# Optimization experiments

Measured on AMD Instinct MI355X. Metric: run time of the kernel, lower is better.

## Reference

```python
import jax, jax.numpy as jnp
import numpy as np

D_MODEL = 1024
NUM_HEADS = 16
LN_EPS = 1e-5


def setup_inputs() -> dict:
    key = jax.random.key(0)
    ks = jax.random.split(key, 8)
    d = D_MODEL
    x = jax.random.normal(ks[0], (8, 1024, d), dtype=jnp.float32)
    # nn.MultiheadAttention parameters (combined in_proj, out_proj)
    in_proj_w = jax.random.normal(ks[1], (3 * d, d), dtype=jnp.float32) / np.sqrt(d)
    in_proj_b = jnp.zeros((3 * d,), dtype=jnp.float32)
    out_proj_w = jax.random.normal(ks[2], (d, d), dtype=jnp.float32) / np.sqrt(d)
    out_proj_b = jnp.zeros((d,), dtype=jnp.float32)
    ln_w = jnp.ones((d,), dtype=jnp.float32)
    ln_b = jnp.zeros((d,), dtype=jnp.float32)
    time_decay = jnp.asarray(0.1, dtype=jnp.float32)
    return {"x": x, "time_decay": time_decay, "in_proj_w": in_proj_w,
            "in_proj_b": in_proj_b, "out_proj_w": out_proj_w,
            "out_proj_b": out_proj_b, "ln_w": ln_w, "ln_b": ln_b}


def reference(x, time_decay, in_proj_w, in_proj_b, out_proj_w, out_proj_b, ln_w, ln_b):
    B, S, d = x.shape
    H = NUM_HEADS
    hd = d // H
    # vectorized time-decay bias: -|time_decay| * |i - j|  (replaces nested loop)
    idx = jnp.arange(S, dtype=jnp.float32)
    attn_bias = -jnp.abs(time_decay) * jnp.abs(idx[:, None] - idx[None, :])  # [S,S]
    # combined QKV projection
    qkv = x @ in_proj_w.T + in_proj_b  # [B,S,3d]
    q, k, v = jnp.split(qkv, 3, axis=-1)
    q = q.reshape(B, S, H, hd)
    k = k.reshape(B, S, H, hd)
    v = v.reshape(B, S, H, hd)
    scale = 1.0 / np.sqrt(hd)
    scores = jnp.einsum('bqhd,bkhd->bhqk', q, k) * scale + attn_bias  # [B,H,S,S]
    weights = jax.nn.softmax(scores, axis=-1)
    attn = jnp.einsum('bhqk,bkhd->bqhd', weights, v).reshape(B, S, d)
    attn_out = attn @ out_proj_w.T + out_proj_b
    # need_weights=True with default average_attn_weights=True -> mean over heads
    attn_weights = jnp.mean(weights, axis=1)  # [B,S,S]
    # residual + LayerNorm
    y = x + attn_out
    mu = jnp.mean(y, axis=-1, keepdims=True)
    var = jnp.mean(jnp.square(y - mu), axis=-1, keepdims=True)
    out = (y - mu) / jnp.sqrt(var + LN_EPS) * ln_w + ln_b
    return (out, attn_weights)
```

## Files before the change

kernel.cpp:

```cpp
#include <hip/hip_runtime.h>
#include <cstddef>

#define BATCH   8
#define SEQ     1024
#define DMODEL  1024
#define NHEAD   16
#define HDIM    64
#define D3      3072
#define NROWS   (BATCH * SEQ)
#define LN_EPS  1e-5f

typedef __attribute__((ext_vector_type(4))) float f32x4;
typedef __attribute__((ext_vector_type(8))) short bf16x8;

__device__ __forceinline__ float b2f(unsigned short u) {
    union { unsigned int i; float f; } v; v.i = ((unsigned int)u) << 16; return v.f;
}
__device__ __forceinline__ unsigned short f2bu(float f) {
    union { float f; unsigned int i; } v; v.f = f;
    unsigned int r = v.i + 0x7fffu + ((v.i >> 16) & 1u);
    return (unsigned short)(r >> 16);
}
__device__ __forceinline__ void gl16(const void* g, void* l) {
    __builtin_amdgcn_global_load_lds(
        (const __attribute__((address_space(1))) unsigned int*)g,
        (__attribute__((address_space(3))) unsigned int*)l, 16, 0, 0);
}

#define NG_X  1048576
#define NG_WQ 393216
#define NG_WO 131072
__global__ __launch_bounds__(256)
void cvt_bf16(const float* __restrict__ x, const float* __restrict__ wq,
              const float* __restrict__ wo,
              unsigned short* __restrict__ xb, unsigned short* __restrict__ wqb,
              unsigned short* __restrict__ wob) {
    const int gidx = blockIdx.x * 256 + threadIdx.x;
    const float* src; unsigned short* dst; size_t off;
    if (gidx < NG_X)              { src = x;  dst = xb;  off = (size_t)gidx * 8; }
    else if (gidx < NG_X + NG_WQ) { src = wq; dst = wqb; off = (size_t)(gidx - NG_X) * 8; }
    else                          { src = wo; dst = wob; off = (size_t)(gidx - NG_X - NG_WQ) * 8; }
    float4 v0 = *(const float4*)(src + off);
    float4 v1 = *(const float4*)(src + off + 4);
    uint4 pv;
    pv.x = f2bu(v0.x) | ((unsigned int)f2bu(v0.y) << 16);
    pv.y = f2bu(v0.z) | ((unsigned int)f2bu(v0.w) << 16);
    pv.z = f2bu(v1.x) | ((unsigned int)f2bu(v1.y) << 16);
    pv.w = f2bu(v1.z) | ((unsigned int)f2bu(v1.w) << 16);
    *(uint4*)(dst + off) = pv;
}

__global__ __launch_bounds__(256)
void qkv_mfma(const unsigned short* __restrict__ xb,
              const unsigned short* __restrict__ wb,
              const float* __restrict__ bias,
              unsigned short* __restrict__ qh,
              unsigned short* __restrict__ kh,
              unsigned short* __restrict__ vt) {
    __shared__ unsigned short smem[8192];
    unsigned short* As = smem;
    unsigned short* Bs = smem + 4096;

    const int t = threadIdx.x;
    const int w = t >> 6, lane = t & 63;
    const int wm = w >> 1, wn = w & 1;
    const int g = lane >> 4, c = lane & 15;
    const int m0 = blockIdx.y * 128, n0 = blockIdx.x * 128;

    const int srow = t >> 2;
    const int scol = (t & 3) * 8;
    const unsigned short* ga = xb + (size_t)(m0 + srow) * 1024 + scol;
    const unsigned short* gb = wb + (size_t)(n0 + srow) * 1024 + scol;

    f32x4 acc[4][4];
#pragma unroll
    for (int i = 0; i < 4; ++i)
#pragma unroll
        for (int j = 0; j < 4; ++j) acc[i][j] = (f32x4){0.f, 0.f, 0.f, 0.f};

    for (int k0 = 0; k0 < 1024; k0 += 32) {
        gl16(ga + k0,             As + t * 8);
        gl16(ga + 64 * 1024 + k0, As + 2048 + t * 8);
        gl16(gb + k0,             Bs + t * 8);
        gl16(gb + 64 * 1024 + k0, Bs + 2048 + t * 8);
        __syncthreads();
        bf16x8 af[4], bf[4];
#pragma unroll
        for (int i = 0; i < 4; ++i)
            af[i] = *(const bf16x8*)(As + (wm * 64 + i * 16 + c) * 32 + g * 8);
#pragma unroll
        for (int j = 0; j < 4; ++j)
            bf[j] = *(const bf16x8*)(Bs + (wn * 64 + j * 16 + c) * 32 + g * 8);
#pragma unroll
        for (int i = 0; i < 4; ++i)
#pragma unroll
            for (int j = 0; j < 4; ++j)
                acc[i][j] = __builtin_amdgcn_mfma_f32_16x16x32_bf16(af[i], bf[j], acc[i][j], 0, 0, 0);
        __syncthreads();
    }

    float bsv[4];
#pragma unroll
    for (int j = 0; j < 4; ++j) bsv[j] = bias[n0 + wn * 64 + j * 16 + c];

    unsigned short* eslice = smem + w * 2048;
    const int b_ = m0 >> 10;

    if (n0 < 2048) {
        const int ncl   = n0 + wn * 64;
        unsigned short* dst = (ncl < 1024)
            ? qh + ((size_t)(b_ * 16 + (ncl >> 6)) * 1024) * 64
            : kh + ((size_t)(b_ * 16 + ((ncl - 1024) >> 6)) * 1024) * 64;
#pragma unroll
        for (int half = 0; half < 2; ++half) {
#pragma unroll
            for (int ii = 0; ii < 2; ++ii) {
                const int i = half * 2 + ii;
#pragma unroll
                for (int j = 0; j < 4; ++j)
#pragma unroll
                    for (int r = 0; r < 4; ++r)
                        eslice[(ii * 16 + g * 4 + r) * 64 + j * 16 + c] = f2bu(acc[i][j][r] + bsv[j]);
            }
#pragma unroll
            for (int u = 0; u < 4; ++u) {
                const int mloc = u * 8 + (lane >> 3);
                const int ncol = (lane & 7) * 8;
                bf16x8 row = *(const bf16x8*)(eslice + mloc * 64 + ncol);
                const int tok = (m0 & 1023) + wm * 64 + half * 32 + mloc;
                *(bf16x8*)(dst + (size_t)tok * 64 + ncol) = row;
            }
        }
    } else {
        const int key0  = (m0 & 1023) + wm * 64;
        const int hbase = (n0 + wn * 64 - 2048) >> 6;
#pragma unroll
        for (int half = 0; half < 2; ++half) {
#pragma unroll
            for (int jj = 0; jj < 2; ++jj) {
                const int j = half * 2 + jj;
                const int nloc = jj * 16 + c;
#pragma unroll
                for (int i = 0; i < 4; ++i)
#pragma unroll
                    for (int r = 0; r < 4; ++r) {
                        const int mloc  = i * 16 + g * 4 + r;
                        const int mphys = mloc ^ ((nloc & 7) << 3);
                        eslice[nloc * 64 + mphys] = f2bu(acc[i][j][r] + bsv[j]);
                    }
            }
#pragma unroll
            for (int u = 0; u < 4; ++u) {
                const int nloc  = u * 8 + (lane >> 3);
                const int mb    = lane & 7;
                const int mphys = (mb ^ (nloc & 7)) * 8;
                bf16x8 row = *(const bf16x8*)(eslice + nloc * 64 + mphys);
                const int d = half * 32 + nloc;
                *(bf16x8*)(vt + ((size_t)((b_ * 16 + hbase) * 64 + d)) * 1024 + key0 + mb * 8) = row;
            }
        }
    }
}

__global__ __launch_bounds__(256, 1)
void attn_mfma(const unsigned short* __restrict__ qh,
               const unsigned short* __restrict__ kh,
               const unsigned short* __restrict__ vt,
               const float* __restrict__ tdp,
               unsigned short* __restrict__ attnb,
               float* __restrict__ wout) {
    const int qt = blockIdx.x;
    const int b  = blockIdx.y;
    const int hg = blockIdx.z;
    const int t  = threadIdx.x;
    const int w  = t >> 6;
    const int lane = t & 63;
    const int g  = lane >> 4;
    const int c  = lane & 15;

    const int q0 = qt * 64;
    const float td2 = -fabsf(tdp[0]) * 1.44269504f;
    const float sc2 = 0.125f * 1.44269504f;

    __shared__ unsigned short P_s[64][1032];
    __shared__ float rs_s[4][64];

    float wsum[4][16][4];
#pragma unroll
    for (int i = 0; i < 4; ++i)
#pragma unroll
        for (int tt = 0; tt < 16; ++tt)
#pragma unroll
            for (int r = 0; r < 4; ++r) wsum[i][tt][r] = 0.f;

    const int key_base = w * 256;
    const float kf0 = (float)(key_base + c);

    for (int hi = 0; hi < 8; ++hi) {
        const int h = hg * 8 + hi;
        const unsigned short* qslab = qh + (size_t)(b * 16 + h) * 1024 * 64;
        const unsigned short* kslab = kh + (size_t)(b * 16 + h) * 1024 * 64;

        bf16x8 qa[4][2];
#pragma unroll
        for (int i = 0; i < 4; ++i) {
            const unsigned short* qp = qslab + (size_t)(q0 + i * 16 + c) * 64 + g * 8;
            qa[i][0] = *(const bf16x8*)(qp);
            qa[i][1] = *(const bf16x8*)(qp + 32);
        }

        float rsum[4][4];
#pragma unroll
        for (int i = 0; i < 4; ++i)
#pragma unroll
            for (int r = 0; r < 4; ++r) rsum[i][r] = 0.f;

#pragma unroll 2
        for (int tt = 0; tt < 16; ++tt) {
            const int key = key_base + tt * 16 + c;
            const unsigned short* kp = kslab + (size_t)key * 64 + g * 8;
            bf16x8 kb0 = *(const bf16x8*)(kp);
            bf16x8 kb1 = *(const bf16x8*)(kp + 32);
            f32x4 z[4];
#pragma unroll
            for (int i = 0; i < 4; ++i) z[i] = (f32x4){0.f, 0.f, 0.f, 0.f};
#pragma unroll
            for (int i = 0; i < 4; ++i)
                z[i] = __builtin_amdgcn_mfma_f32_16x16x32_bf16(qa[i][0], kb0, z[i], 0, 0, 0);
#pragma unroll
            for (int i = 0; i < 4; ++i)
                z[i] = __builtin_amdgcn_mfma_f32_16x16x32_bf16(qa[i][1], kb1, z[i], 0, 0, 0);
            const float kf = kf0 + (float)(tt * 16);
#pragma unroll
            for (int i = 0; i < 4; ++i) {
#pragma unroll
                for (int r = 0; r < 4; ++r) {
                    const float qf = (float)(q0 + i * 16 + g * 4 + r);
                    const float e = __builtin_amdgcn_exp2f(z[i][r] * sc2 + td2 * fabsf(kf - qf));
                    rsum[i][r] += e;
                    P_s[i * 16 + g * 4 + r][key_base + tt * 16 + c] = f2bu(e);
                }
            }
        }
#pragma unroll
        for (int i = 0; i < 4; ++i)
#pragma unroll
            for (int r = 0; r < 4; ++r) {
                rsum[i][r] += __shfl_xor(rsum[i][r], 1, 64);
                rsum[i][r] += __shfl_xor(rsum[i][r], 2, 64);
                rsum[i][r] += __shfl_xor(rsum[i][r], 4, 64);
                rsum[i][r] += __shfl_xor(rsum[i][r], 8, 64);
            }
        if (c == 0) {
#pragma unroll
            for (int i = 0; i < 4; ++i)
#pragma unroll
                for (int r = 0; r < 4; ++r) rs_s[w][i * 16 + g * 4 + r] = rsum[i][r];
        }
        __syncthreads();

        float invl[4][4];
#pragma unroll
        for (int i = 0; i < 4; ++i)
#pragma unroll
            for (int r = 0; r < 4; ++r) {
                const int row = i * 16 + g * 4 + r;
                invl[i][r] = 1.0f / (rs_s[0][row] + rs_s[1][row] + rs_s[2][row] + rs_s[3][row]);
            }

        f32x4 accO[4];
#pragma unroll
        for (int i = 0; i < 4; ++i) accO[i] = (f32x4){0.f, 0.f, 0.f, 0.f};
        const unsigned short* vhp = vt + (size_t)((b * 16 + h) * 64 + w * 16 + c) * 1024;
#pragma unroll 4
        for (int ks = 0; ks < 32; ++ks) {
            bf16x8 vb = *(const bf16x8*)(vhp + ks * 32 + g * 8);
#pragma unroll
            for (int i = 0; i < 4; ++i) {
                bf16x8 pa = *(const bf16x8*)(&P_s[i * 16 + c][ks * 32 + g * 8]);
                accO[i] = __builtin_amdgcn_mfma_f32_16x16x32_bf16(pa, vb, accO[i], 0, 0, 0);
            }
        }
        {
            unsigned short* op = attnb + (size_t)(b * 1024 + q0) * 1024 + h * 64 + w * 16 + c;
#pragma unroll
            for (int i = 0; i < 4; ++i)
#pragma unroll
                for (int r = 0; r < 4; ++r)
                    op[(size_t)(i * 16 + g * 4 + r) * 1024] = f2bu(accO[i][r] * invl[i][r]);
        }

#pragma unroll
        for (int i = 0; i < 4; ++i)
#pragma unroll
            for (int tt = 0; tt < 16; ++tt)
#pragma unroll
                for (int r = 0; r < 4; ++r)
                    wsum[i][tt][r] += b2f(P_s[i * 16 + g * 4 + r][key_base + tt * 16 + c]) * invl[i][r];
        __syncthreads();
    }

#pragma unroll
    for (int i = 0; i < 4; ++i)
#pragma unroll
        for (int tt = 0; tt < 16; ++tt)
#pragma unroll
            for (int r = 0; r < 4; ++r) {
                atomicAdd(&wout[(size_t)(b * 1024 + q0 + i * 16 + g * 4 + r) * 1024
                                 + key_base + tt * 16 + c],
                          wsum[i][tt][r] * (1.0f / NHEAD));
            }
}

__global__ __launch_bounds__(256)
void outproj_mfma(const unsigned short* __restrict__ ab,
                  const unsigned short* __restrict__ wob,
                  const float* __restrict__ bias,
                  const float* __restrict__ X,
                  float* __restrict__ Y) {
    __shared__ unsigned short smem[8192];
    unsigned short* As = smem;
    unsigned short* Bs = smem + 4096;

    const int t = threadIdx.x;
    const int w = t >> 6, lane = t & 63;
    const int wm = w >> 1, wn = w & 1;
    const int g = lane >> 4, c = lane & 15;
    const int m0 = blockIdx.y * 128, n0 = blockIdx.x * 128;

    const int srow = t >> 2;
    const int scol = (t & 3) * 8;
    const unsigned short* ga = ab  + (size_t)(m0 + srow) * 1024 + scol;
    const unsigned short* gb = wob + (size_t)(n0 + srow) * 1024 + scol;

    f32x4 acc[4][4];
#pragma unroll
    for (int i = 0; i < 4; ++i)
#pragma unroll
        for (int j = 0; j < 4; ++j) acc[i][j] = (f32x4){0.f, 0.f, 0.f, 0.f};

    for (int k0 = 0; k0 < 1024; k0 += 32) {
        gl16(ga + k0,             As + t * 8);
        gl16(ga + 64 * 1024 + k0, As + 2048 + t * 8);
        gl16(gb + k0,             Bs + t * 8);
        gl16(gb + 64 * 1024 + k0, Bs + 2048 + t * 8);
        __syncthreads();
        bf16x8 af[4], bf[4];
#pragma unroll
        for (int i = 0; i < 4; ++i)
            af[i] = *(const bf16x8*)(As + (wm * 64 + i * 16 + c) * 32 + g * 8);
#pragma unroll
        for (int j = 0; j < 4; ++j)
            bf[j] = *(const bf16x8*)(Bs + (wn * 64 + j * 16 + c) * 32 + g * 8);
#pragma unroll
        for (int i = 0; i < 4; ++i)
#pragma unroll
            for (int j = 0; j < 4; ++j)
                acc[i][j] = __builtin_amdgcn_mfma_f32_16x16x32_bf16(af[i], bf[j], acc[i][j], 0, 0, 0);
        __syncthreads();
    }

    float bsv[4];
#pragma unroll
    for (int j = 0; j < 4; ++j) bsv[j] = bias[n0 + wn * 64 + j * 16 + c];

#pragma unroll
    for (int i = 0; i < 4; ++i) {
#pragma unroll
        for (int r = 0; r < 4; ++r) {
            const int m = m0 + wm * 64 + i * 16 + g * 4 + r;
#pragma unroll
            for (int j = 0; j < 4; ++j) {
                const int n = n0 + wn * 64 + j * 16 + c;
                Y[(size_t)m * 1024 + n] = acc[i][j][r] + bsv[j] + X[(size_t)m * 1024 + n];
            }
        }
    }
}

__global__ __launch_bounds__(256)
void ln_kernel(const float* __restrict__ Y, const float* __restrict__ lnw,
               const float* __restrict__ lnb, float* __restrict__ out) {
    const int row = blockIdx.x, t = threadIdx.x;
    __shared__ float rs[256], rq[256];
    const float4 v = ((const float4*)(Y + (size_t)row * DMODEL))[t];
    rs[t] = v.x + v.y + v.z + v.w;
    rq[t] = v.x * v.x + v.y * v.y + v.z * v.z + v.w * v.w;
    __syncthreads();
    for (int off = 128; off > 0; off >>= 1) {
        if (t < off) { rs[t] += rs[t + off]; rq[t] += rq[t + off]; }
        __syncthreads();
    }
    const float mu   = rs[0] * (1.0f / DMODEL);
    const float var  = rq[0] * (1.0f / DMODEL) - mu * mu;
    const float rstd = rsqrtf(var + LN_EPS);
    const float4 w  = ((const float4*)lnw)[t];
    const float4 bb = ((const float4*)lnb)[t];
    float4 o;
    o.x = (v.x - mu) * rstd * w.x + bb.x;
    o.y = (v.y - mu) * rstd * w.y + bb.y;
    o.z = (v.z - mu) * rstd * w.z + bb.z;
    o.w = (v.w - mu) * rstd * w.w + bb.w;
    ((float4*)(out + (size_t)row * DMODEL))[t] = o;
}

extern "C" void kernel_launch(void* const* d_in, const int* in_sizes, int n_in,
                              void* d_out, int out_size, void* d_ws, size_t ws_size,
                              hipStream_t stream) {
    (void)in_sizes; (void)n_in; (void)out_size; (void)ws_size;
    const float* x    = (const float*)d_in[0];
    const float* td   = (const float*)d_in[1];
    const float* wqkv = (const float*)d_in[2];
    const float* bqkv = (const float*)d_in[3];
    const float* wo   = (const float*)d_in[4];
    const float* bo   = (const float*)d_in[5];
    const float* lnw  = (const float*)d_in[6];
    const float* lnb  = (const float*)d_in[7];

    float* out_ln = (float*)d_out;
    float* out_w  = (float*)d_out + (size_t)NROWS * SEQ;

    unsigned short* qh = (unsigned short*)d_ws;
    unsigned short* kh = qh + (size_t)128 * 1024 * 64;
    unsigned short* vt = kh + (size_t)128 * 1024 * 64;
    float*          y  = (float*)d_ws;

    unsigned short* attnb = (unsigned short*)d_out;
    unsigned short* wob   = (unsigned short*)d_out + (size_t)NROWS * DMODEL;
    unsigned short* xb    = (unsigned short*)out_w;
    unsigned short* wqkvb = xb + (size_t)NROWS * DMODEL;

    cvt_bf16    <<<(NG_X + NG_WQ + NG_WO) / 256, 256, 0, stream>>>(x, wqkv, wo, xb, wqkvb, wob);
    qkv_mfma    <<<dim3(D3 / 128, NROWS / 128), 256, 0, stream>>>(xb, wqkvb, bqkv, qh, kh, vt);
    (void)hipMemsetAsync(out_w, 0, (size_t)BATCH * SEQ * SEQ * sizeof(float), stream);
    attn_mfma   <<<dim3(SEQ / 64, BATCH, 2),    256, 0, stream>>>(qh, kh, vt, td, attnb, out_w);
    outproj_mfma<<<dim3(DMODEL / 128, NROWS / 128), 256, 0, stream>>>(attnb, wob, bo, x, y);
    ln_kernel   <<<NROWS,                       256, 0, stream>>>(y, lnw, lnb, out_ln);
}
```

Baseline: 483.3 us.

## Use 8 waves per attention block with split-K PV and LDS reduction

The attention kernel moves from 256 to 512 threads per block. Each wave now covers 128 keys instead of 256, which halves the per-thread wsum register array. For the PV product, waves split the key dimension into two halves and combine their partial outputs through an LDS reduction buffer. The goal is more waves in flight and lower register pressure, at the cost of extra syncthreads, extra LDS, and the reduction step.

```diff
diff --git a/kernel.cpp b/kernel.cpp
--- a/kernel.cpp
+++ b/kernel.cpp
@@ -162,7 +162,7 @@
     }
 }
 
-__global__ __launch_bounds__(256, 1)
+__global__ __launch_bounds__(512, 2)
 void attn_mfma(const unsigned short* __restrict__ qh,
                const unsigned short* __restrict__ kh,
                const unsigned short* __restrict__ vt,
@@ -183,17 +183,19 @@
     const float sc2 = 0.125f * 1.44269504f;
 
     __shared__ unsigned short P_s[64][1032];
-    __shared__ float rs_s[4][64];
-
-    float wsum[4][16][4];
+    __shared__ float rs_s[8][64];
+    __shared__ float rs_tot[64];
+    __shared__ float Ored[4][4][16][17];
+
+    float wsum[4][8][4];
 #pragma unroll
     for (int i = 0; i < 4; ++i)
 #pragma unroll
-        for (int tt = 0; tt < 16; ++tt)
+        for (int tt = 0; tt < 8; ++tt)
 #pragma unroll
             for (int r = 0; r < 4; ++r) wsum[i][tt][r] = 0.f;
 
-    const int key_base = w * 256;
+    const int key_base = w * 128;
     const float kf0 = (float)(key_base + c);
 
     for (int hi = 0; hi < 8; ++hi) {
@@ -216,7 +218,7 @@
             for (int r = 0; r < 4; ++r) rsum[i][r] = 0.f;
 
 #pragma unroll 2
-        for (int tt = 0; tt < 16; ++tt) {
+        for (int tt = 0; tt < 8; ++tt) {
             const int key = key_base + tt * 16 + c;
             const unsigned short* kp = kslab + (size_t)key * 64 + g * 8;
             bf16x8 kb0 = *(const bf16x8*)(kp);
@@ -259,21 +261,29 @@
         }
         __syncthreads();
 
+        if (t < 64) {
+            float s = 0.f;
+#pragma unroll
+            for (int j = 0; j < 8; ++j) s += rs_s[j][t];
+            rs_tot[t] = 1.0f / s;
+        }
+        __syncthreads();
+
         float invl[4][4];
 #pragma unroll
         for (int i = 0; i < 4; ++i)
 #pragma unroll
-            for (int r = 0; r < 4; ++r) {
-                const int row = i * 16 + g * 4 + r;
-                invl[i][r] = 1.0f / (rs_s[0][row] + rs_s[1][row] + rs_s[2][row] + rs_s[3][row]);
-            }
-
+            for (int r = 0; r < 4; ++r)
+                invl[i][r] = rs_tot[i * 16 + g * 4 + r];
+
+        const int dsl = (w & 3) * 16;
+        const int ks0 = (w >> 2) * 16;
         f32x4 accO[4];
 #pragma unroll
         for (int i = 0; i < 4; ++i) accO[i] = (f32x4){0.f, 0.f, 0.f, 0.f};
-        const unsigned short* vhp = vt + (size_t)((b * 16 + h) * 64 + w * 16 + c) * 1024;
+        const unsigned short* vhp = vt + (size_t)((b * 16 + h) * 64 + dsl + c) * 1024;
 #pragma unroll 4
-        for (int ks = 0; ks < 32; ++ks) {
+        for (int ks = ks0; ks < ks0 + 16; ++ks) {
             bf16x8 vb = *(const bf16x8*)(vhp + ks * 32 + g * 8);
 #pragma unroll
             for (int i = 0; i < 4; ++i) {
@@ -281,19 +291,29 @@
                 accO[i] = __builtin_amdgcn_mfma_f32_16x16x32_bf16(pa, vb, accO[i], 0, 0, 0);
             }
         }
-        {
-            unsigned short* op = attnb + (size_t)(b * 1024 + q0) * 1024 + h * 64 + w * 16 + c;
+        if (w >= 4) {
 #pragma unroll
             for (int i = 0; i < 4; ++i)
 #pragma unroll
                 for (int r = 0; r < 4; ++r)
-                    op[(size_t)(i * 16 + g * 4 + r) * 1024] = f2bu(accO[i][r] * invl[i][r]);
-        }
-
-#pragma unroll
-        for (int i = 0; i < 4; ++i)
-#pragma unroll
-            for (int tt = 0; tt < 16; ++tt)
+                    Ored[w - 4][i][g * 4 + r][c] = accO[i][r];
+        }
+        __syncthreads();
+        if (w < 4) {
+            unsigned short* op = attnb + (size_t)(b * 1024 + q0) * 1024 + h * 64 + dsl + c;
+#pragma unroll
+            for (int i = 0; i < 4; ++i)
+#pragma unroll
+                for (int r = 0; r < 4; ++r) {
+                    const float o = accO[i][r] + Ored[w][i][g * 4 + r][c];
+                    op[(size_t)(i * 16 + g * 4 + r) * 1024] = f2bu(o * invl[i][r]);
+                }
+        }
+
+#pragma unroll
+        for (int i = 0; i < 4; ++i)
+#pragma unroll
+            for (int tt = 0; tt < 8; ++tt)
 #pragma unroll
                 for (int r = 0; r < 4; ++r)
                     wsum[i][tt][r] += b2f(P_s[i * 16 + g * 4 + r][key_base + tt * 16 + c]) * invl[i][r];
@@ -303,7 +323,7 @@
 #pragma unroll
     for (int i = 0; i < 4; ++i)
 #pragma unroll
-        for (int tt = 0; tt < 16; ++tt)
+        for (int tt = 0; tt < 8; ++tt)
 #pragma unroll
             for (int r = 0; r < 4; ++r) {
                 atomicAdd(&wout[(size_t)(b * 1024 + q0 + i * 16 + g * 4 + r) * 1024
@@ -347,7 +367,7 @@
         __syncthreads();
         bf16x8 af[4], bf[4];
 #pragma unroll
-        for (int i = 0; i < 4; ++i)
+    for (int i = 0; i < 4; ++i)
             af[i] = *(const bf16x8*)(As + (wm * 64 + i * 16 + c) * 32 + g * 8);
 #pragma unroll
         for (int j = 0; j < 4; ++j)
@@ -433,7 +453,7 @@
     cvt_bf16    <<<(NG_X + NG_WQ + NG_WO) / 256, 256, 0, stream>>>(x, wqkv, wo, xb, wqkvb, wob);
     qkv_mfma    <<<dim3(D3 / 128, NROWS / 128), 256, 0, stream>>>(xb, wqkvb, bqkv, qh, kh, vt);
     (void)hipMemsetAsync(out_w, 0, (size_t)BATCH * SEQ * SEQ * sizeof(float), stream);
-    attn_mfma   <<<dim3(SEQ / 64, BATCH, 2),    256, 0, stream>>>(qh, kh, vt, td, attnb, out_w);
+    attn_mfma   <<<dim3(SEQ / 64, BATCH, 2),    512, 0, stream>>>(qh, kh, vt, td, attnb, out_w);
     outproj_mfma<<<dim3(DMODEL / 128, NROWS / 128), 256, 0, stream>>>(attnb, wob, bo, x, y);
     ln_kernel   <<<NROWS,                       256, 0, stream>>>(y, lnw, lnb, out_ln);
 }
```

Result: faster. 424.6 us (-12.1%).
